# Performance work log

Hardware: AMD Instinct MI355X
Metric: run time of the kernel (lower is better)

Reference implementation:

```python
import jax, jax.numpy as jnp
import numpy as np

B, L, DIM = 8, 512, 8          # batch, seq len, raw channels (value dim D = 2*DIM = 16)
ET, HID, H = 128, 128, 2       # embed_time, hidden_size, num_heads
MAXLEN = 512
NEG = -1e9


def setup_inputs() -> dict:
    key = jax.random.key(0)
    ks = jax.random.split(key, 40)
    def n(i, shape, s=0.05):
        return jax.random.normal(ks[i], shape, jnp.float32) * s
    vals = jax.random.normal(ks[0], (B, L, DIM), jnp.float32)
    msk = (jax.random.uniform(ks[1], (B, L, DIM)) > 0.2).astype(jnp.float32)
    x = jnp.concatenate([vals, msk], -1)                      # (B, L, 2*DIM)
    time_steps = jax.random.uniform(ks[2], (B, L), jnp.float32)
    return {
        'x': x, 'time_steps': time_steps,
        # learned time embedding: Linear(1, ET-1) periodic + Linear(1,1)
        'w_per': n(3, (1, ET - 1)), 'b_per': n(4, (ET - 1,)),
        'w_lin': n(5, (1, 1)), 'b_lin': n(6, (1,)),
        # MultiTimeAttention projections
        'Wq_t': n(7, (ET, ET)), 'bq_t': n(8, (ET,)),
        'Wk_t': n(9, (ET, ET)), 'bk_t': n(10, (ET,)),
        'Wo_t': n(11, (2 * DIM * H, HID)), 'bo_t': n(12, (HID,)),
        'pos_emb': n(13, (MAXLEN + 1, HID)), 'cls_emb': n(14, (1, HID)),
        # transformer block (BERT-style post-LN encoder layer, d_ff=HID)
        'tWq': n(15, (HID, HID)), 'tbq': n(16, (HID,)),
        'tWk': n(17, (HID, HID)), 'tbk': n(18, (HID,)),
        'tWv': n(19, (HID, HID)), 'tbv': n(20, (HID,)),
        'tWo': n(21, (HID, HID)), 'tbo': n(22, (HID,)),
        'ln1_g': jnp.ones((HID,), jnp.float32), 'ln1_b': jnp.zeros((HID,), jnp.float32),
        'fW1': n(23, (HID, HID)), 'fb1': n(24, (HID,)),
        'fW2': n(25, (HID, HID)), 'fb2': n(26, (HID,)),
        'ln2_g': jnp.ones((HID,), jnp.float32), 'ln2_b': jnp.zeros((HID,), jnp.float32),
        # BertPooler
        'pW': n(27, (HID, HID)), 'pb': n(28, (HID,)),
    }


def _time_emb(tt, w_per, b_per, w_lin, b_lin):
    tt = tt[..., None]                                        # (B, L, 1)
    return jnp.concatenate([tt @ w_lin + b_lin, jnp.sin(tt @ w_per + b_per)], -1)


def _ln(x, g, b, eps=1e-5):
    m = x.mean(-1, keepdims=True)
    v = ((x - m) ** 2).mean(-1, keepdims=True)
    return (x - m) / jnp.sqrt(v + eps) * g + b


def _mta(q_emb, k_emb, value, mask, Wq, bq, Wk, bk, Wo, bo):
    # MultiTimeAttention: scores broadcast to value-channel axis, softmax over keys
    D = value.shape[-1]
    dk = ET // H
    def split(e, W, b):
        p = e @ W + b
        return p.reshape(e.shape[0], -1, H, dk).transpose(0, 2, 1, 3)
    q = split(q_emb, Wq, bq)                                  # (Bq, H, Lq, dk)
    k = split(k_emb, Wk, bk)                                  # (B,  H, Lk, dk)
    scores = jnp.matmul(q, k.swapaxes(-1, -2)) / jnp.sqrt(jnp.float32(dk))  # (B,H,Lq,Lk)
    s5 = jnp.where(mask[:, None, None, :, :] == 0, NEG, scores[..., None])  # (B,H,Lq,Lk,D)
    p = jax.nn.softmax(s5, axis=-2)
    out = jnp.einsum('bhqkd,bkd->bhqd', p, value)             # (B, H, Lq, D)
    Bv = value.shape[0]
    out = out.transpose(0, 2, 1, 3).reshape(Bv, -1, H * D)
    return out @ Wo + bo


def _tblock(x, tWq, tbq, tWk, tbk, tWv, tbv, tWo, tbo, ln1_g, ln1_b,
            fW1, fb1, fW2, fb2, ln2_g, ln2_b):
    Bq, Lq, _ = x.shape
    dk = HID // H
    def heads(W, b):
        return (x @ W + b).reshape(Bq, Lq, H, dk).transpose(0, 2, 1, 3)
    q, k, v = heads(tWq, tbq), heads(tWk, tbk), heads(tWv, tbv)
    a = jax.nn.softmax(jnp.matmul(q, k.swapaxes(-1, -2)) / jnp.sqrt(jnp.float32(dk)), -1)
    o = jnp.matmul(a, v).transpose(0, 2, 1, 3).reshape(Bq, Lq, HID) @ tWo + tbo
    x = _ln(x + o, ln1_g, ln1_b)
    f = jax.nn.relu(x @ fW1 + fb1) @ fW2 + fb2
    return _ln(x + f, ln2_g, ln2_b)


def reference(x, time_steps, w_per, b_per, w_lin, b_lin,
              Wq_t, bq_t, Wk_t, bk_t, Wo_t, bo_t, pos_emb, cls_emb,
              tWq, tbq, tWk, tbk, tWv, tbv, tWo, tbo, ln1_g, ln1_b,
              fW1, fb1, fW2, fb2, ln2_g, ln2_b, pW, pb):
    Bx = x.shape[0]
    mask_half = x[:, :, DIM:]
    mask = jnp.concatenate([mask_half, mask_half], -1)        # (B, L, 2*DIM)
    key_e = _time_emb(time_steps, w_per, b_per, w_lin, b_lin)
    tq_e = _time_emb(time_steps, w_per, b_per, w_lin, b_lin)  # query_time_steps=None -> same
    cls_t = jnp.linspace(0.0, 1.0, 128, dtype=jnp.float32)[None]
    cls_q_e = _time_emb(cls_t, w_per, b_per, w_lin, b_lin)    # (1, 128, ET)
    cls_out = _mta(cls_q_e, key_e, x, mask, Wq_t, bq_t, Wk_t, bk_t, Wo_t, bo_t)
    out = _mta(tq_e, key_e, x, mask, Wq_t, bq_t, Wk_t, bk_t, Wo_t, bo_t)
    tb = (tWq, tbq, tWk, tbk, tWv, tbv, tWo, tbo, ln1_g, ln1_b,
          fW1, fb1, fW2, fb2, ln2_g, ln2_b)
    cls_repr = jnp.broadcast_to(cls_emb[None, :, :], (Bx, 1, HID))
    # encode(cls_out, is_pooling=True), pooling='bert': no pos emb, take token 0
    h = _tblock(jnp.concatenate([cls_repr, cls_out], 1), *tb)
    cls_pooling = jnp.tanh(h[:, 0] @ pW + pb)                 # (B, HID)
    # encode(out, is_pooling=False) [pretrain path]: pos emb + transformer, drop CLS
    h2 = jnp.concatenate([cls_repr, out], 1)                  # (B, L+1, HID)
    h2 = h2 + pos_emb[:h2.shape[1]][None]
    h2 = _tblock(h2, *tb)
    last_hidden_state = h2[:, 1:]                             # (B, L, HID)
    return cls_pooling, last_hidden_state
```

## Files before the change

kernel.cpp:

```cpp
#include <hip/hip_runtime.h>
#include <hip/hip_bf16.h>
#include <math.h>


static constexpr int NM_ = 8 * 513;
static constexpr int NC_ = 8 * 129;
static constexpr int NT_ = NM_ + NC_;

using bf = __hip_bfloat16;
typedef __attribute__((ext_vector_type(8))) short bf16x8;
typedef __attribute__((ext_vector_type(4))) short bf16x4;
typedef __attribute__((ext_vector_type(4))) float floatx4;
typedef __attribute__((ext_vector_type(8))) unsigned short ushortx8;

__device__ __forceinline__ float wave_reduce_sum(float v) {
    #pragma unroll
    for (int off = 32; off >= 1; off >>= 1) v += __shfl_xor(v, off);
    return v;
}
__device__ __forceinline__ float wave_reduce_max(float v) {
    #pragma unroll
    for (int off = 32; off >= 1; off >>= 1) v = fmaxf(v, __shfl_xor(v, off));
    return v;
}
__device__ __forceinline__ float u2f(unsigned short u) {
    return __uint_as_float(((unsigned)u) << 16);
}
__device__ __forceinline__ unsigned short f2u(float f) {
    unsigned u = __float_as_uint(f);
    return (unsigned short)((u + 0x7FFF + ((u >> 16) & 1)) >> 16);
}
__device__ __forceinline__ bf16x8 join8(bf16x4 lo, bf16x4 hi) {
    return __builtin_shufflevector(lo, hi, 0, 1, 2, 3, 4, 5, 6, 7);
}
__device__ __forceinline__ float rdin(const void* p, int i, int flag) {
    return flag ? u2f(((const unsigned short*)p)[i]) : ((const float*)p)[i];
}

struct PrepAll {
    const void* src[32]; int n[32]; int dstoff[32];
    int cstart[32]; int cnum[32];
    int ncv;
    const void* wsrc[8]; unsigned short* wdst[8]; float wscale[8];
    const void* ts; const void* w_per; const void* b_per;
    const void* w_lin; const void* b_lin;
    unsigned short* key_e16;
    unsigned short* btg;
    const void* xsrc;
    const unsigned short* det;
};
__global__ void prep_all_kernel(PrepAll a, float* dst) {
    int flag = (a.det[0] == 0x3F80u) ? 1 : 0;
    int blk = blockIdx.x, tid = threadIdx.x;
    if (blk < a.ncv) {
        int which = -1, bi = 0;
        #pragma unroll
        for (int i = 0; i < 32; ++i)
            if (blk >= a.cstart[i] && blk < a.cstart[i] + a.cnum[i]) { which = i; bi = blk - a.cstart[i]; }
        if (which < 0) return;
        int i = bi * 256 + tid;
        if (i < a.n[which]) dst[a.dstoff[which] + i] = rdin(a.src[which], i, flag);
    } else if (blk < a.ncv + 512) {
        int p = blk - a.ncv;
        int m = p >> 6;
        int idx = (p & 63) * 256 + tid;
        int c = idx >> 9;
        int l = (idx >> 3) & 63;
        int j = idx & 7;
        int k = (c >> 3) * 32 + (l >> 4) * 8 + j;
        int n = (c & 7) * 16 + (l & 15);
        a.wdst[m][idx] = f2u(rdin(a.wsrc[m], k * 128 + n, flag) * a.wscale[m]);
    } else if (blk < a.ncv + 512 + 2112) {
        int p = blk - a.ncv - 512;
        int row = p * 2 + (tid >> 7), j = tid & 127;
        float t = (row < 4096) ? rdin(a.ts, row, flag)
                               : (float)(row - 4096) * (1.0f / 127.0f);
        float v;
        if (j == 0) v = t * rdin(a.w_lin, 0, flag) + rdin(a.b_lin, 0, flag);
        else        v = sinf(t * rdin(a.w_per, j - 1, flag) + rdin(a.b_per, j - 1, flag));
        a.key_e16[row * 128 + j] = f2u(v);
    } else {
        int p = blk - a.ncv - 512 - 2112;
        int e0 = (p * 256 + tid) * 8;
        int b = e0 >> 13;
        int c = (e0 >> 9) & 15;
        int k0 = e0 & 511;
        unsigned short out[8];
        #pragma unroll
        for (int j = 0; j < 8; ++j) {
            int k = k0 + j;
            float m = rdin(a.xsrc, (b * 512 + k) * 16 + 8 + (c & 7), flag);
            float val = (c < 8) ? rdin(a.xsrc, (b * 512 + k) * 16 + c, flag) * m : m;
            out[j] = f2u(val);
        }
        *(ushortx8*)(a.btg + e0) = *(ushortx8*)out;
    }
}

struct GemmM {
    const void* A[3]; const unsigned short* W[3]; const float* bias[3];
    unsigned short* C[3];
    int M[3]; float bscale[3];
};
__global__ void __launch_bounds__(256)
gemm_mfma_kernel(GemmM p) {
    int y = blockIdx.y;
    const unsigned short* Wsw = p.W[y];
    const float* bias = p.bias[y];
    unsigned short* C = p.C[y];
    int M = p.M[y];
    float bscale = p.bscale[y];
    int m0 = blockIdx.x * 16;
    if (m0 >= M) return;
    __shared__ unsigned short As[16][136];
    int tid = threadIdx.x;
    {
        const unsigned short* A = (const unsigned short*)p.A[y];
        int r = tid >> 4, c0 = (tid & 15) * 8;
        ushortx8 v = {0, 0, 0, 0, 0, 0, 0, 0};
        if (m0 + r < M) v = *(const ushortx8*)(A + (size_t)(m0 + r) * 128 + c0);
        *(ushortx8*)&As[r][c0] = v;
    }
    __syncthreads();

    int wv = tid >> 6, lane = tid & 63;
    floatx4 acc0 = {0.f, 0.f, 0.f, 0.f}, acc1 = acc0;
    int am = lane & 15, aq = lane >> 4;
    #pragma unroll
    for (int ks = 0; ks < 4; ++ks) {
        bf16x8 af = *(bf16x8*)&As[am][ks * 32 + aq * 8];
        const unsigned short* base = Wsw + ((size_t)ks * 8 + 2 * wv) * 512 + lane * 8;
        bf16x8 b0 = *(const bf16x8*)(base);
        bf16x8 b1 = *(const bf16x8*)(base + 512);
        acc0 = __builtin_amdgcn_mfma_f32_16x16x32_bf16(af, b0, acc0, 0, 0, 0);
        acc1 = __builtin_amdgcn_mfma_f32_16x16x32_bf16(af, b1, acc1, 0, 0, 0);
    }
    int col = lane & 15, rowb = (lane >> 4) * 4;
    #pragma unroll
    for (int t = 0; t < 2; ++t) {
        floatx4 acc = t ? acc1 : acc0;
        int n = wv * 32 + t * 16 + col;
        float bv = bias[n] * bscale;
        #pragma unroll
        for (int rg = 0; rg < 4; ++rg) {
            int m = m0 + rowb + rg;
            if (m < M) C[(size_t)m * 128 + n] = f2u(acc[rg] + bv);
        }
    }
}

__global__ void __launch_bounds__(256)
mta_att_kernel(const unsigned short* qp_cls, const unsigned short* qp_main,
               const unsigned short* kp, const unsigned short* btg,
               float* att_cls, float* att_mn) {
    int is_cls = (blockIdx.x >= 32);
    int qt = is_cls ? (blockIdx.x - 32) : blockIdx.x;
    int h = blockIdx.y, b = blockIdx.z;
    int tid = threadIdx.x, lane = tid & 63, wv = tid >> 6;
    __shared__ unsigned short Qs[16][72];
    __shared__ unsigned short KV[64][72];
    __shared__ unsigned short sp[16][520];
    int q0 = qt * 16;

    if (tid < 128) {
        int r = tid >> 3, c0 = (tid & 7) * 8;
        const unsigned short* qrow = is_cls ? (qp_cls + (size_t)(q0 + r) * 128 + h * 64)
                                            : (qp_main + (size_t)(b * 512 + q0 + r) * 128 + h * 64);
        *(ushortx8*)&Qs[r][c0] = *(const ushortx8*)(qrow + c0);
    }
    __syncthreads();

    bf16x8 qf0, qf1;
    {
        int m = lane & 15, g = lane >> 4;
        qf0 = *(const bf16x8*)&Qs[m][g * 8];
        qf1 = *(const bf16x8*)&Qs[m][32 + g * 8];
    }

    for (int kt = 0; kt < 8; ++kt) {
        int k0 = kt * 64;
        {
            int kk = tid >> 3, e0 = (tid & 7) * 8;
            #pragma unroll
            for (int it = 0; it < 2; ++it, kk += 32)
                *(ushortx8*)&KV[kk][e0] =
                    *(const ushortx8*)(kp + (size_t)(b * 512 + k0 + kk) * 128 + h * 64 + e0);
        }
        __syncthreads();
        int kn = lane & 15, g = lane >> 4;
        floatx4 acc = {0.f, 0.f, 0.f, 0.f};
        {
            bf16x8 b0 = *(const bf16x8*)&KV[wv * 16 + kn][g * 8];
            acc = __builtin_amdgcn_mfma_f32_16x16x32_bf16(qf0, b0, acc, 0, 0, 0);
            bf16x8 b1 = *(const bf16x8*)&KV[wv * 16 + kn][32 + g * 8];
            acc = __builtin_amdgcn_mfma_f32_16x16x32_bf16(qf1, b1, acc, 0, 0, 0);
        }
        int colk = k0 + wv * 16 + kn;
        #pragma unroll
        for (int rg = 0; rg < 4; ++rg) sp[g * 4 + rg][colk] = f2u(acc[rg]);
        __syncthreads();
    }

    for (int rr = wv; rr < 16; rr += 4) {
        float m = -1e30f;
        for (int k = lane; k < 512; k += 64) m = fmaxf(m, u2f(sp[rr][k]));
        m = wave_reduce_max(m);
        for (int k = lane; k < 512; k += 64) sp[rr][k] = f2u(expf(u2f(sp[rr][k]) - m));
    }
    __syncthreads();

    floatx4 macc = {0.f, 0.f, 0.f, 0.f};
    {
        int mq = lane & 15, g = lane >> 4;
        const unsigned short* bbase = btg + ((size_t)(b * 16 + mq)) * 512 + g * 8;
        #pragma unroll
        for (int cc = 0; cc < 4; ++cc) {
            int koff = (wv + cc * 4) * 32;
            bf16x8 af = *(const bf16x8*)&sp[mq][koff + g * 8];
            bf16x8 bfv = *(const bf16x8*)(bbase + koff);
            macc = __builtin_amdgcn_mfma_f32_16x16x32_bf16(af, bfv, macc, 0, 0, 0);
        }
    }
    float* redC = (float*)&KV[0][0];
    float* Cfull = redC + 1024;
    #pragma unroll
    for (int rg = 0; rg < 4; ++rg) redC[(wv * 64 + lane) * 4 + rg] = macc[rg];
    __syncthreads();
    {
        int l = tid >> 2, rg = tid & 3;
        float s = redC[l * 4 + rg] + redC[(64 + l) * 4 + rg]
                + redC[(128 + l) * 4 + rg] + redC[(192 + l) * 4 + rg];
        int row = (l >> 4) * 4 + rg, c = l & 15;
        Cfull[row * 16 + c] = s;
    }
    __syncthreads();
    if (tid < 128) {
        int r = tid >> 3, c = tid & 7;
        float num = Cfull[r * 16 + c];
        float den = Cfull[r * 16 + 8 + c];
        int row = q0 + r;
        float* dst = is_cls ? (att_cls + (size_t)(b * 128 + row) * 32)
                            : (att_mn + (size_t)(b * 512 + row) * 32);
        dst[h * 16 + c] = num / den;
        dst[h * 16 + 8 + c] = 1.0f;
    }
}

__global__ void __launch_bounds__(256)
mta_qkv_kernel(const float* att, const float* Wo, const float* bo,
               const float* cls_emb, const float* pos, float* xin,
               const unsigned short* Wq, const unsigned short* Wk, const unsigned short* Wv,
               const float* bq, const float* bk, const float* bv_,
               unsigned short* outq, unsigned short* outk, unsigned short* outv) {
    int m0 = blockIdx.x * 16;
    __shared__ float As32[16][36];
    __shared__ unsigned short As[16][136];
    int tid = threadIdx.x;
    int r = tid >> 4, g = tid & 15, c0 = g * 8;

    int R = m0 + r;
    int srow, prow;
    if (R < NM_) {
        int b = R / 513, rr = R - b * 513;
        srow = (rr == 0) ? -1 : 1024 + b * 512 + (rr - 1);
        prow = rr;
    } else {
        int mc = R - NM_;
        int b = mc / 129, rr = mc - b * 129;
        srow = (rr == 0) ? -1 : b * 128 + (rr - 1);
        prow = -1;
    }
    if (g < 2 && srow >= 0) {
        const float* src = att + (size_t)srow * 32 + g * 16;
        *(float4*)&As32[r][g * 16]      = *(const float4*)(src);
        *(float4*)&As32[r][g * 16 + 4]  = *(const float4*)(src + 4);
        *(float4*)&As32[r][g * 16 + 8]  = *(const float4*)(src + 8);
        *(float4*)&As32[r][g * 16 + 12] = *(const float4*)(src + 12);
    }
    __syncthreads();

    float acc[8];
    if (srow < 0) {
        #pragma unroll
        for (int j = 0; j < 8; ++j) acc[j] = cls_emb[c0 + j];
    } else {
        #pragma unroll
        for (int j = 0; j < 8; ++j) acc[j] = bo[c0 + j];
        #pragma unroll 8
        for (int k = 0; k < 32; ++k) {
            float a = As32[r][k];
            const float4 w0 = *(const float4*)(Wo + (size_t)k * 128 + c0);
            const float4 w1 = *(const float4*)(Wo + (size_t)k * 128 + c0 + 4);
            acc[0] = fmaf(a, w0.x, acc[0]); acc[1] = fmaf(a, w0.y, acc[1]);
            acc[2] = fmaf(a, w0.z, acc[2]); acc[3] = fmaf(a, w0.w, acc[3]);
            acc[4] = fmaf(a, w1.x, acc[4]); acc[5] = fmaf(a, w1.y, acc[5]);
            acc[6] = fmaf(a, w1.z, acc[6]); acc[7] = fmaf(a, w1.w, acc[7]);
        }
    }
    if (prow >= 0) {
        const float* pr = pos + (size_t)prow * 128 + c0;
        float4 p0 = *(const float4*)(pr);
        float4 p1 = *(const float4*)(pr + 4);
        acc[0] += p0.x; acc[1] += p0.y; acc[2] += p0.z; acc[3] += p0.w;
        acc[4] += p1.x; acc[5] += p1.y; acc[6] += p1.z; acc[7] += p1.w;
    }
    *(float4*)(xin + (size_t)R * 128 + c0) = make_float4(acc[0], acc[1], acc[2], acc[3]);
    *(float4*)(xin + (size_t)R * 128 + c0 + 4) = make_float4(acc[4], acc[5], acc[6], acc[7]);
    *(ushort4*)&As[r][c0] = make_ushort4(f2u(acc[0]), f2u(acc[1]), f2u(acc[2]), f2u(acc[3]));
    *(ushort4*)&As[r][c0 + 4] = make_ushort4(f2u(acc[4]), f2u(acc[5]), f2u(acc[6]), f2u(acc[7]));
    __syncthreads();

    int wv = tid >> 6, lane = tid & 63;
    int am = lane & 15, aq = lane >> 4;
    int col = lane & 15, rowb = (lane >> 4) * 4;
    const unsigned short* Ws[3] = {Wq, Wk, Wv};
    const float* bs[3] = {bq, bk, bv_};
    float bsc[3] = {0.125f, 1.f, 1.f};
    unsigned short* Cs[3] = {outq, outk, outv};
    #pragma unroll
    for (int y = 0; y < 3; ++y) {
        floatx4 acc0 = {0.f, 0.f, 0.f, 0.f}, acc1 = acc0;
        #pragma unroll
        for (int ks = 0; ks < 4; ++ks) {
            bf16x8 af = *(bf16x8*)&As[am][ks * 32 + aq * 8];
            const unsigned short* base = Ws[y] + ((size_t)ks * 8 + 2 * wv) * 512 + lane * 8;
            bf16x8 b0 = *(const bf16x8*)(base);
            bf16x8 b1 = *(const bf16x8*)(base + 512);
            acc0 = __builtin_amdgcn_mfma_f32_16x16x32_bf16(af, b0, acc0, 0, 0, 0);
            acc1 = __builtin_amdgcn_mfma_f32_16x16x32_bf16(af, b1, acc1, 0, 0, 0);
        }
        #pragma unroll
        for (int t = 0; t < 2; ++t) {
            floatx4 a2 = t ? acc1 : acc0;
            int n = wv * 32 + t * 16 + col;
            float bvv = bs[y][n] * bsc[y];
            #pragma unroll
            for (int rg = 0; rg < 4; ++rg)
                Cs[y][(size_t)(m0 + rowb + rg) * 128 + n] = f2u(a2[rg] + bvv);
        }
    }
}

__global__ void __launch_bounds__(256)
tb_att_kernel(const unsigned short* qp, const unsigned short* kp,
              const unsigned short* vp, unsigned short* outp) {
    int is_cls = (blockIdx.x >= 33);
    int qt = is_cls ? blockIdx.x - 33 : blockIdx.x;
    int h = blockIdx.y, b = blockIdx.z;
    int Lq = is_cls ? 129 : 513;
    int base = is_cls ? (4104 + b * 129) : (b * 513);
    int nkt = is_cls ? 3 : 9;
    int tid = threadIdx.x, lane = tid & 63, wv = tid >> 6;
    __shared__ unsigned short Qs[16][72];
    __shared__ unsigned short KV[64][72];
    __shared__ unsigned short sp[16][588];
    __shared__ float rinv[16];
    int q0 = qt * 16;

    if (tid < 128) {
        int r = tid >> 3, c0 = (tid & 7) * 8;
        int qr = q0 + r;
        ushortx8 v = {0, 0, 0, 0, 0, 0, 0, 0};
        if (qr < Lq) v = *(const ushortx8*)(qp + (size_t)(base + qr) * 128 + h * 64 + c0);
        *(ushortx8*)&Qs[r][c0] = v;
    }
    __syncthreads();

    bf16x8 qf0, qf1;
    {
        int m = lane & 15, g = lane >> 4;
        qf0 = *(const bf16x8*)&Qs[m][g * 8];
        qf1 = *(const bf16x8*)&Qs[m][32 + g * 8];
    }

    for (int kt = 0; kt < nkt; ++kt) {
        int k0 = kt * 64;
        {
            int kk = tid >> 3, e0 = (tid & 7) * 8;
            #pragma unroll
            for (int it = 0; it < 2; ++it, kk += 32) {
                int krow = k0 + kk;
                ushortx8 v = {0, 0, 0, 0, 0, 0, 0, 0};
                if (krow < Lq) v = *(const ushortx8*)(kp + (size_t)(base + krow) * 128 + h * 64 + e0);
                *(ushortx8*)&KV[kk][e0] = v;
            }
        }
        __syncthreads();
        int kn = lane & 15, g = lane >> 4;
        floatx4 acc = {0.f, 0.f, 0.f, 0.f};
        {
            bf16x8 b0 = *(const bf16x8*)&KV[wv * 16 + kn][g * 8];
            acc = __builtin_amdgcn_mfma_f32_16x16x32_bf16(qf0, b0, acc, 0, 0, 0);
            bf16x8 b1 = *(const bf16x8*)&KV[wv * 16 + kn][32 + g * 8];
            acc = __builtin_amdgcn_mfma_f32_16x16x32_bf16(qf1, b1, acc, 0, 0, 0);
        }
        int colk = k0 + wv * 16 + kn;
        #pragma unroll
        for (int rg = 0; rg < 4; ++rg)
            sp[g * 4 + rg][colk] = f2u((colk < Lq) ? acc[rg] : -1e30f);
        __syncthreads();
    }

    int kend = nkt * 64;
    for (int rr = wv; rr < 16; rr += 4) {
        float m = -1e30f;
        for (int k = lane; k < kend; k += 64) m = fmaxf(m, u2f(sp[rr][k]));
        m = wave_reduce_max(m);
        float sum = 0.f;
        for (int k = lane; k < kend; k += 64) {
            float e = expf(u2f(sp[rr][k]) - m);
            sp[rr][k] = f2u(e);
            sum += e;
        }
        sum = wave_reduce_sum(sum);
        if (lane == 0) rinv[rr] = 1.f / sum;
    }

    floatx4 oacc = {0.f, 0.f, 0.f, 0.f};
    for (int kt = 0; kt < nkt; ++kt) {
        int k0 = kt * 64;
        __syncthreads();
        {
            int kk = tid & 31, e0 = (tid >> 5) * 8;
            #pragma unroll
            for (int it = 0; it < 2; ++it, kk += 32) {
                int krow = k0 + kk;
                ushortx8 v = {0, 0, 0, 0, 0, 0, 0, 0};
                if (krow < Lq) v = *(const ushortx8*)(vp + (size_t)(base + krow) * 128 + h * 64 + e0);
                #pragma unroll
                for (int j = 0; j < 8; ++j) KV[e0 + j][kk] = v[j];
            }
        }
        __syncthreads();
        int dn = lane & 15, g = lane >> 4;
        #pragma unroll
        for (int c = 0; c < 2; ++c) {
            bf16x4 plo = *(const bf16x4*)&sp[lane & 15][k0 + c * 32 + g * 8];
            bf16x4 phi = *(const bf16x4*)&sp[lane & 15][k0 + c * 32 + g * 8 + 4];
            bf16x8 vf = *(const bf16x8*)&KV[wv * 16 + dn][c * 32 + g * 8];
            oacc = __builtin_amdgcn_mfma_f32_16x16x32_bf16(join8(plo, phi), vf, oacc, 0, 0, 0);
        }
    }
    int dcol = wv * 16 + (lane & 15), g = lane >> 4;
    #pragma unroll
    for (int rg = 0; rg < 4; ++rg) {
        int q = g * 4 + rg;
        int qr = q0 + q;
        if (qr < Lq)
            outp[(size_t)(base + qr) * 128 + h * 64 + dcol] = f2u(oacc[rg] * rinv[q]);
    }
}

__global__ void __launch_bounds__(256)
attnout_ffn_kernel(const unsigned short* A, const unsigned short* Wao, const float* bao,
                   const float* resid, const float* g1, const float* b1ln,
                   const unsigned short* W1, const float* fb1,
                   const unsigned short* W2, const float* fb2,
                   const float* g2, const float* b2ln,
                   const float* pW, const float* pb, float* dout) {
    int m0 = blockIdx.x * 16;
    __shared__ unsigned short As[16][136];
    __shared__ float Xs[16][128];
    __shared__ unsigned short Hs[16][136];
    __shared__ float redS[4][4][4], redQ[4][4][4];
    __shared__ float smean[16], sinv[16];
    __shared__ float x2row[128];
    __shared__ int poolb;
    int tid = threadIdx.x;
    if (tid == 0) poolb = -1;
    {
        int r = tid >> 4, c0 = (tid & 15) * 8;
        *(ushortx8*)&As[r][c0] = *(const ushortx8*)(A + (size_t)(m0 + r) * 128 + c0);
    }
    __syncthreads();

    int wv = tid >> 6, lane = tid & 63;
    int am = lane & 15, aq = lane >> 4;
    int col = lane & 15, g = lane >> 4, rowb = g * 4;

    float ov[2][4];
    {
        floatx4 acc0 = {0.f, 0.f, 0.f, 0.f}, acc1 = acc0;
        #pragma unroll
        for (int ks = 0; ks < 4; ++ks) {
            bf16x8 af = *(bf16x8*)&As[am][ks * 32 + aq * 8];
            const unsigned short* base = Wao + ((size_t)ks * 8 + 2 * wv) * 512 + lane * 8;
            bf16x8 bb0 = *(const bf16x8*)(base);
            bf16x8 bb1 = *(const bf16x8*)(base + 512);
            acc0 = __builtin_amdgcn_mfma_f32_16x16x32_bf16(af, bb0, acc0, 0, 0, 0);
            acc1 = __builtin_amdgcn_mfma_f32_16x16x32_bf16(af, bb1, acc1, 0, 0, 0);
        }
        #pragma unroll
        for (int t = 0; t < 2; ++t) {
            int n = wv * 32 + t * 16 + col;
            float bv = bao[n];
            floatx4 acc = t ? acc1 : acc0;
            #pragma unroll
            for (int rg = 0; rg < 4; ++rg)
                ov[t][rg] = acc[rg] + bv + resid[(size_t)(m0 + rowb + rg) * 128 + n];
        }
    }
    #pragma unroll
    for (int rg = 0; rg < 4; ++rg) {
        float s = ov[0][rg] + ov[1][rg];
        float q = ov[0][rg] * ov[0][rg] + ov[1][rg] * ov[1][rg];
        #pragma unroll
        for (int off = 8; off >= 1; off >>= 1) {
            s += __shfl_xor(s, off);
            q += __shfl_xor(q, off);
        }
        if ((lane & 15) == 0) { redS[wv][g][rg] = s; redQ[wv][g][rg] = q; }
    }
    __syncthreads();
    if (tid < 16) {
        int gg = tid >> 2, rg = tid & 3;
        float s = redS[0][gg][rg] + redS[1][gg][rg] + redS[2][gg][rg] + redS[3][gg][rg];
        float q = redQ[0][gg][rg] + redQ[1][gg][rg] + redQ[2][gg][rg] + redQ[3][gg][rg];
        float mean = s * 0.0078125f;
        float var = q * 0.0078125f - mean * mean;
        smean[tid] = mean;
        sinv[tid] = rsqrtf(var + 1e-5f);
    }
    __syncthreads();
    #pragma unroll
    for (int t = 0; t < 2; ++t) {
        int n = wv * 32 + t * 16 + col;
        float gm = g1[n], bb = b1ln[n];
        #pragma unroll
        for (int rg = 0; rg < 4; ++rg) {
            int row = rowb + rg;
            float val = (ov[t][rg] - smean[row]) * sinv[row] * gm + bb;
            Xs[row][n] = val;
            As[row][n] = f2u(val);
        }
    }
    __syncthreads();

    {
        floatx4 acc0 = {0.f, 0.f, 0.f, 0.f}, acc1 = acc0;
        #pragma unroll
        for (int ks = 0; ks < 4; ++ks) {
            bf16x8 af = *(bf16x8*)&As[am][ks * 32 + aq * 8];
            const unsigned short* base = W1 + ((size_t)ks * 8 + 2 * wv) * 512 + lane * 8;
            bf16x8 bb0 = *(const bf16x8*)(base);
            bf16x8 bb1 = *(const bf16x8*)(base + 512);
            acc0 = __builtin_amdgcn_mfma_f32_16x16x32_bf16(af, bb0, acc0, 0, 0, 0);
            acc1 = __builtin_amdgcn_mfma_f32_16x16x32_bf16(af, bb1, acc1, 0, 0, 0);
        }
        #pragma unroll
        for (int t = 0; t < 2; ++t) {
            int n = wv * 32 + t * 16 + col;
            float bv = fb1[n];
            floatx4 acc = t ? acc1 : acc0;
            #pragma unroll
            for (int rg = 0; rg < 4; ++rg)
                Hs[rowb + rg][n] = f2u(fmaxf(acc[rg] + bv, 0.f));
        }
    }
    __syncthreads();

    floatx4 acc0 = {0.f, 0.f, 0.f, 0.f}, acc1 = acc0;
    #pragma unroll
    for (int ks = 0; ks < 4; ++ks) {
        bf16x8 af = *(bf16x8*)&Hs[am][ks * 32 + aq * 8];
        const unsigned short* base = W2 + ((size_t)ks * 8 + 2 * wv) * 512 + lane * 8;
        bf16x8 bb0 = *(const bf16x8*)(base);
        bf16x8 bb1 = *(const bf16x8*)(base + 512);
        acc0 = __builtin_amdgcn_mfma_f32_16x16x32_bf16(af, bb0, acc0, 0, 0, 0);
        acc1 = __builtin_amdgcn_mfma_f32_16x16x32_bf16(af, bb1, acc1, 0, 0, 0);
    }
    #pragma unroll
    for (int t = 0; t < 2; ++t) {
        int n = wv * 32 + t * 16 + col;
        float bv = fb2[n];
        floatx4 acc = t ? acc1 : acc0;
        #pragma unroll
        for (int rg = 0; rg < 4; ++rg)
            ov[t][rg] = acc[rg] + bv + Xs[rowb + rg][n];
    }
    #pragma unroll
    for (int rg = 0; rg < 4; ++rg) {
        float s = ov[0][rg] + ov[1][rg];
        float q = ov[0][rg] * ov[0][rg] + ov[1][rg] * ov[1][rg];
        #pragma unroll
        for (int off = 8; off >= 1; off >>= 1) {
            s += __shfl_xor(s, off);
            q += __shfl_xor(q, off);
        }
        if ((lane & 15) == 0) { redS[wv][g][rg] = s; redQ[wv][g][rg] = q; }
    }
    __syncthreads();
    if (tid < 16) {
        int gg = tid >> 2, rg = tid & 3;
        float s = redS[0][gg][rg] + redS[1][gg][rg] + redS[2][gg][rg] + redS[3][gg][rg];
        float q = redQ[0][gg][rg] + redQ[1][gg][rg] + redQ[2][gg][rg] + redQ[3][gg][rg];
        float mean = s * 0.0078125f;
        float var = q * 0.0078125f - mean * mean;
        smean[tid] = mean;
        sinv[tid] = rsqrtf(var + 1e-5f);
    }
    __syncthreads();
    #pragma unroll
    for (int t = 0; t < 2; ++t) {
        int n = wv * 32 + t * 16 + col;
        float gm = g2[n], bb = b2ln[n];
        #pragma unroll
        for (int rg = 0; rg < 4; ++rg) {
            int row = rowb + rg;
            int m = m0 + row;
            float val = (ov[t][rg] - smean[row]) * sinv[row] * gm + bb;
            if (m < NM_) {
                int b = m / 513, r = m - b * 513;
                if (r >= 1)
                    dout[1024 + (size_t)b * 65536 + (size_t)(r - 1) * 128 + n] = val;
            } else {
                int mc = m - NM_;
                int b = mc / 129, r = mc - b * 129;
                if (r == 0) {
                    x2row[n] = val;
                    if (n == 0) poolb = b;
                }
            }
        }
    }
    __syncthreads();
    if (poolb >= 0 && tid < 128) {
        float acc = pb[tid];
        for (int k = 0; k < 128; ++k) acc = fmaf(x2row[k], pW[(size_t)k * 128 + tid], acc);
        dout[(size_t)poolb * 128 + tid] = tanhf(acc);
    }
}

extern "C" void kernel_launch(void* const* d_in, const int* in_sizes, int n_in,
                              void* d_out, int out_size, void* d_ws, size_t ws_size,
                              hipStream_t stream) {
    float* w = (float*)d_ws;
    size_t off = 0;
    auto alloc = [&](size_t n) {
        float* p = w + off;
        off += (n + 3) & ~(size_t)3;
        return p;
    };
    auto allocU = [&](size_t n) { return (unsigned short*)alloc((n + 1) / 2); };

    PrepAll pa{};
    int nn = n_in < 32 ? n_in : 32;
    float* fin[32];
    const int needconv[32] = {0,0,0,0,0,0, 0,1, 0,1, 1,1, 1,1, 0,1, 0,1, 0,1,
                              0,1, 1,1, 0,1, 0,1, 1,1, 1,1};
    int ncv = 0;
    for (int i = 0; i < nn; ++i) {
        pa.src[i] = d_in[i];
        pa.n[i] = in_sizes[i];
        fin[i] = alloc(in_sizes[i]);
        pa.dstoff[i] = (int)(fin[i] - w);
        if (needconv[i]) {
            int nb = (in_sizes[i] + 255) / 256;
            pa.cstart[i] = ncv;
            pa.cnum[i] = nb;
            ncv += nb;
        } else { pa.cstart[i] = -1; pa.cnum[i] = 0; }
    }
    for (int i = nn; i < 32; ++i) {
        pa.src[i] = nullptr; pa.n[i] = 0; pa.dstoff[i] = 0;
        pa.cstart[i] = -1; pa.cnum[i] = 0;
    }
    pa.ncv = ncv;

    const float* bq_t    = fin[7];
    const float* bk_t    = fin[9];
    const float* Wo_t    = fin[10]; const float* bo_t = fin[11];
    const float* pos_emb = fin[12]; const float* cls_emb = fin[13];
    const float* tbq = fin[15]; const float* tbk = fin[17]; const float* tbv = fin[19];
    const float* tbo = fin[21];
    const float* ln1_g = fin[22]; const float* ln1_b = fin[23];
    const float* fb1 = fin[25]; const float* fb2 = fin[27];
    const float* ln2_g = fin[28]; const float* ln2_b = fin[29];
    const float* pW = fin[30]; const float* pb = fin[31];

    const int widx[8] = {8, 6, 14, 16, 18, 20, 24, 26};
    unsigned short* wsw[8];
    for (int i = 0; i < 8; ++i) {
        wsw[i] = allocU(16384);
        pa.wsrc[i] = d_in[widx[i]];
        pa.wdst[i] = wsw[i];
        pa.wscale[i] = (i == 1 || i == 2) ? 0.125f : 1.0f;
    }
    pa.ts = d_in[1]; pa.w_per = d_in[2]; pa.b_per = d_in[3];
    pa.w_lin = d_in[4]; pa.b_lin = d_in[5];
    pa.xsrc = d_in[0];
    pa.det = (const unsigned short*)d_in[22];

    unsigned short* key_e16 = allocU(4224 * 128);
    unsigned short* cls_e16 = key_e16 + 4096 * 128;
    pa.key_e16 = key_e16;
    unsigned short* btg = allocU(8 * 16 * 512);
    pa.btg = btg;

    unsigned short* qp_main16 = allocU(4096 * 128);
    unsigned short* kp_main16 = allocU(4096 * 128);
    unsigned short* qp_cls16  = allocU(128 * 128);
    float* att_all = alloc(5120 * 32);
    float* att_cls = att_all;
    float* att_mn  = att_all + 1024 * 32;
    float* xin     = alloc((size_t)NT_ * 128);
    unsigned short* tbq16 = allocU((size_t)NT_ * 128);
    unsigned short* tbk16 = allocU((size_t)NT_ * 128);
    unsigned short* tbv16 = allocU((size_t)NT_ * 128);
    unsigned short* tba16 = allocU((size_t)NT_ * 128);
    (void)ws_size;

    float* outf = (float*)d_out;

    prep_all_kernel<<<ncv + 512 + 2112 + 32, 256, 0, stream>>>(pa, w);

    {
        GemmM p{};
        p.A[0] = key_e16; p.W[0] = wsw[0]; p.bias[0] = bk_t; p.C[0] = kp_main16;
        p.M[0] = 4096; p.bscale[0] = 1.f;
        p.A[1] = key_e16; p.W[1] = wsw[1]; p.bias[1] = bq_t; p.C[1] = qp_main16;
        p.M[1] = 4096; p.bscale[1] = 0.125f;
        p.A[2] = cls_e16; p.W[2] = wsw[1]; p.bias[2] = bq_t; p.C[2] = qp_cls16;
        p.M[2] = 128; p.bscale[2] = 0.125f;
        gemm_mfma_kernel<<<dim3(256, 3), 256, 0, stream>>>(p);
    }

    mta_att_kernel<<<dim3(40, 2, 8), 256, 0, stream>>>(qp_cls16, qp_main16, kp_main16,
                                                       btg, att_cls, att_mn);

    mta_qkv_kernel<<<321, 256, 0, stream>>>(att_all, Wo_t, bo_t, cls_emb, pos_emb, xin,
                                            wsw[2], wsw[3], wsw[4], tbq, tbk, tbv,
                                            tbq16, tbk16, tbv16);

    tb_att_kernel<<<dim3(42, 2, 8), 256, 0, stream>>>(tbq16, tbk16, tbv16, tba16);

    attnout_ffn_kernel<<<321, 256, 0, stream>>>(tba16, wsw[5], tbo, xin, ln1_g, ln1_b,
                                                wsw[6], fb1, wsw[7], fb2, ln2_g, ln2_b,
                                                pW, pb, outf);
}
```

Before: 180.4 us.

## Store V transposed and load MFMA operands directly from global memory

The QKV projection kernel now writes V transposed into a padded buffer, with a strided layout and zeroed tail columns set up in the prep kernel. The transformer attention kernel then reads V fragments straight from global memory instead of staging and transposing them through LDS. The GEMM, MTA attention and transformer attention kernels also load Q and K fragments directly from global memory, which removes the LDS staging and many __syncthreads per tile. In exchange, the transposed V write is a scattered, uncoalesced store, and the direct loads depend on cache hits rather than shared-memory reuse.

```diff
diff --git a/kernel.cpp b/kernel.cpp
--- a/kernel.cpp
+++ b/kernel.cpp
@@ -6,6 +6,7 @@
 static constexpr int NM_ = 8 * 513;
 static constexpr int NC_ = 8 * 129;
 static constexpr int NT_ = NM_ + NC_;
+static constexpr int VTS_ = 5248;
 
 using bf = __hip_bfloat16;
 typedef __attribute__((ext_vector_type(8))) short bf16x8;
@@ -47,6 +48,7 @@
     unsigned short* key_e16;
     unsigned short* btg;
     const void* xsrc;
+    unsigned short* vt;
     const unsigned short* det;
 };
 __global__ void prep_all_kernel(PrepAll a, float* dst) {
@@ -79,7 +81,7 @@
         if (j == 0) v = t * rdin(a.w_lin, 0, flag) + rdin(a.b_lin, 0, flag);
         else        v = sinf(t * rdin(a.w_per, j - 1, flag) + rdin(a.b_per, j - 1, flag));
         a.key_e16[row * 128 + j] = f2u(v);
-    } else {
+    } else if (blk < a.ncv + 512 + 2112 + 32) {
         int p = blk - a.ncv - 512 - 2112;
         int e0 = (p * 256 + tid) * 8;
         int b = e0 >> 13;
@@ -94,6 +96,12 @@
             out[j] = f2u(val);
         }
         *(ushortx8*)(a.btg + e0) = *(ushortx8*)out;
+    } else {
+        int p = blk - a.ncv - 512 - 2112 - 32;
+        int idx = p * 256 + tid;
+        int n = idx / 14, c8 = idx - n * 14;
+        ushortx8 z = {0, 0, 0, 0, 0, 0, 0, 0};
+        *(ushortx8*)(a.vt + (size_t)n * VTS_ + 5136 + c8 * 8) = z;
     }
 }
 
@@ -112,23 +120,15 @@
     float bscale = p.bscale[y];
     int m0 = blockIdx.x * 16;
     if (m0 >= M) return;
-    __shared__ unsigned short As[16][136];
     int tid = threadIdx.x;
-    {
-        const unsigned short* A = (const unsigned short*)p.A[y];
-        int r = tid >> 4, c0 = (tid & 15) * 8;
-        ushortx8 v = {0, 0, 0, 0, 0, 0, 0, 0};
-        if (m0 + r < M) v = *(const ushortx8*)(A + (size_t)(m0 + r) * 128 + c0);
-        *(ushortx8*)&As[r][c0] = v;
-    }
-    __syncthreads();
-
     int wv = tid >> 6, lane = tid & 63;
+    int am = lane & 15, aq = lane >> 4;
+    const unsigned short* A = (const unsigned short*)p.A[y];
+    const unsigned short* Arow = A + (size_t)(m0 + am) * 128;
     floatx4 acc0 = {0.f, 0.f, 0.f, 0.f}, acc1 = acc0;
-    int am = lane & 15, aq = lane >> 4;
     #pragma unroll
     for (int ks = 0; ks < 4; ++ks) {
-        bf16x8 af = *(bf16x8*)&As[am][ks * 32 + aq * 8];
+        bf16x8 af = *(const bf16x8*)(Arow + ks * 32 + aq * 8);
         const unsigned short* base = Wsw + ((size_t)ks * 8 + 2 * wv) * 512 + lane * 8;
         bf16x8 b0 = *(const bf16x8*)(base);
         bf16x8 b1 = *(const bf16x8*)(base + 512);
@@ -142,10 +142,8 @@
         int n = wv * 32 + t * 16 + col;
         float bv = bias[n] * bscale;
         #pragma unroll
-        for (int rg = 0; rg < 4; ++rg) {
-            int m = m0 + rowb + rg;
-            if (m < M) C[(size_t)m * 128 + n] = f2u(acc[rg] + bv);
-        }
+        for (int rg = 0; rg < 4; ++rg)
+            C[(size_t)(m0 + rowb + rg) * 128 + n] = f2u(acc[rg] + bv);
     }
 }
 
@@ -157,74 +155,54 @@
     int qt = is_cls ? (blockIdx.x - 32) : blockIdx.x;
     int h = blockIdx.y, b = blockIdx.z;
     int tid = threadIdx.x, lane = tid & 63, wv = tid >> 6;
-    __shared__ unsigned short Qs[16][72];
-    __shared__ unsigned short KV[64][72];
     __shared__ unsigned short sp[16][520];
+    __shared__ float red[1024 + 256];
     int q0 = qt * 16;
-
-    if (tid < 128) {
-        int r = tid >> 3, c0 = (tid & 7) * 8;
-        const unsigned short* qrow = is_cls ? (qp_cls + (size_t)(q0 + r) * 128 + h * 64)
-                                            : (qp_main + (size_t)(b * 512 + q0 + r) * 128 + h * 64);
-        *(ushortx8*)&Qs[r][c0] = *(const ushortx8*)(qrow + c0);
-    }
-    __syncthreads();
-
-    bf16x8 qf0, qf1;
-    {
-        int m = lane & 15, g = lane >> 4;
-        qf0 = *(const bf16x8*)&Qs[m][g * 8];
-        qf1 = *(const bf16x8*)&Qs[m][32 + g * 8];
-    }
-
+    int m = lane & 15, g = lane >> 4;
+
+    const unsigned short* qrow = is_cls ? (qp_cls + (size_t)(q0 + m) * 128 + h * 64)
+                                        : (qp_main + (size_t)(b * 512 + q0 + m) * 128 + h * 64);
+    bf16x8 qf0 = *(const bf16x8*)(qrow + g * 8);
+    bf16x8 qf1 = *(const bf16x8*)(qrow + 32 + g * 8);
+
+    const unsigned short* kbase = kp + ((size_t)b * 512) * 128 + h * 64;
+    #pragma unroll
     for (int kt = 0; kt < 8; ++kt) {
-        int k0 = kt * 64;
-        {
-            int kk = tid >> 3, e0 = (tid & 7) * 8;
-            #pragma unroll
-            for (int it = 0; it < 2; ++it, kk += 32)
-                *(ushortx8*)&KV[kk][e0] =
-                    *(const ushortx8*)(kp + (size_t)(b * 512 + k0 + kk) * 128 + h * 64 + e0);
-        }
-        __syncthreads();
-        int kn = lane & 15, g = lane >> 4;
+        int colk = kt * 64 + wv * 16 + m;
+        const unsigned short* kb = kbase + (size_t)colk * 128;
+        bf16x8 b0 = *(const bf16x8*)(kb + g * 8);
+        bf16x8 b1 = *(const bf16x8*)(kb + 32 + g * 8);
         floatx4 acc = {0.f, 0.f, 0.f, 0.f};
-        {
-            bf16x8 b0 = *(const bf16x8*)&KV[wv * 16 + kn][g * 8];
-            acc = __builtin_amdgcn_mfma_f32_16x16x32_bf16(qf0, b0, acc, 0, 0, 0);
-            bf16x8 b1 = *(const bf16x8*)&KV[wv * 16 + kn][32 + g * 8];
-            acc = __builtin_amdgcn_mfma_f32_16x16x32_bf16(qf1, b1, acc, 0, 0, 0);
-        }
-        int colk = k0 + wv * 16 + kn;
+        acc = __builtin_amdgcn_mfma_f32_16x16x32_bf16(qf0, b0, acc, 0, 0, 0);
+        acc = __builtin_amdgcn_mfma_f32_16x16x32_bf16(qf1, b1, acc, 0, 0, 0);
         #pragma unroll
         for (int rg = 0; rg < 4; ++rg) sp[g * 4 + rg][colk] = f2u(acc[rg]);
-        __syncthreads();
-    }
+    }
+    __syncthreads();
 
     for (int rr = wv; rr < 16; rr += 4) {
-        float m = -1e30f;
-        for (int k = lane; k < 512; k += 64) m = fmaxf(m, u2f(sp[rr][k]));
-        m = wave_reduce_max(m);
-        for (int k = lane; k < 512; k += 64) sp[rr][k] = f2u(expf(u2f(sp[rr][k]) - m));
+        float mx = -1e30f;
+        for (int k = lane; k < 512; k += 64) mx = fmaxf(mx, u2f(sp[rr][k]));
+        mx = wave_reduce_max(mx);
+        for (int k = lane; k < 512; k += 64) sp[rr][k] = f2u(expf(u2f(sp[rr][k]) - mx));
     }
     __syncthreads();
 
     floatx4 macc = {0.f, 0.f, 0.f, 0.f};
     {
-        int mq = lane & 15, g = lane >> 4;
-        const unsigned short* bbase = btg + ((size_t)(b * 16 + mq)) * 512 + g * 8;
+        const unsigned short* bbase = btg + ((size_t)(b * 16 + m)) * 512 + g * 8;
         #pragma unroll
         for (int cc = 0; cc < 4; ++cc) {
             int koff = (wv + cc * 4) * 32;
-            bf16x8 af = *(const bf16x8*)&sp[mq][koff + g * 8];
+            bf16x8 af = *(const bf16x8*)&sp[m][koff + g * 8];
             bf16x8 bfv = *(const bf16x8*)(bbase + koff);
             macc = __builtin_amdgcn_mfma_f32_16x16x32_bf16(af, bfv, macc, 0, 0, 0);
         }
     }
-    float* redC = (float*)&KV[0][0];
-    float* Cfull = redC + 1024;
-    #pragma unroll
-    for (int rg = 0; rg < 4; ++rg) redC[(wv * 64 + lane) * 4 + rg] = macc[rg];
+    float* redC = red;
+    float* Cfull = red + 1024;
+    #pragma unroll
+    for (int rg = 0; rg < 4; ++rg) redC[tid * 4 + rg] = macc[rg];
     __syncthreads();
     {
         int l = tid >> 2, rg = tid & 3;
@@ -251,7 +229,7 @@
                const float* cls_emb, const float* pos, float* xin,
                const unsigned short* Wq, const unsigned short* Wk, const unsigned short* Wv,
                const float* bq, const float* bk, const float* bv_,
-               unsigned short* outq, unsigned short* outk, unsigned short* outv) {
+               unsigned short* outq, unsigned short* outk, unsigned short* vT) {
     int m0 = blockIdx.x * 16;
     __shared__ float As32[16][36];
     __shared__ unsigned short As[16][136];
@@ -316,7 +294,7 @@
     const unsigned short* Ws[3] = {Wq, Wk, Wv};
     const float* bs[3] = {bq, bk, bv_};
     float bsc[3] = {0.125f, 1.f, 1.f};
-    unsigned short* Cs[3] = {outq, outk, outv};
+    unsigned short* Cs[2] = {outq, outk};
     #pragma unroll
     for (int y = 0; y < 3; ++y) {
         floatx4 acc0 = {0.f, 0.f, 0.f, 0.f}, acc1 = acc0;
@@ -335,15 +313,18 @@
             int n = wv * 32 + t * 16 + col;
             float bvv = bs[y][n] * bsc[y];
             #pragma unroll
-            for (int rg = 0; rg < 4; ++rg)
-                Cs[y][(size_t)(m0 + rowb + rg) * 128 + n] = f2u(a2[rg] + bvv);
+            for (int rg = 0; rg < 4; ++rg) {
+                unsigned short val = f2u(a2[rg] + bvv);
+                if (y < 2) Cs[y][(size_t)(m0 + rowb + rg) * 128 + n] = val;
+                else       vT[(size_t)n * VTS_ + (m0 + rowb + rg)] = val;
+            }
         }
     }
 }
 
 __global__ void __launch_bounds__(256)
 tb_att_kernel(const unsigned short* qp, const unsigned short* kp,
-              const unsigned short* vp, unsigned short* outp) {
+              const unsigned short* vT, unsigned short* outp) {
     int is_cls = (blockIdx.x >= 33);
     int qt = is_cls ? blockIdx.x - 33 : blockIdx.x;
     int h = blockIdx.y, b = blockIdx.z;
@@ -351,103 +332,66 @@
     int base = is_cls ? (4104 + b * 129) : (b * 513);
     int nkt = is_cls ? 3 : 9;
     int tid = threadIdx.x, lane = tid & 63, wv = tid >> 6;
-    __shared__ unsigned short Qs[16][72];
-    __shared__ unsigned short KV[64][72];
     __shared__ unsigned short sp[16][588];
     __shared__ float rinv[16];
     int q0 = qt * 16;
-
-    if (tid < 128) {
-        int r = tid >> 3, c0 = (tid & 7) * 8;
-        int qr = q0 + r;
-        ushortx8 v = {0, 0, 0, 0, 0, 0, 0, 0};
-        if (qr < Lq) v = *(const ushortx8*)(qp + (size_t)(base + qr) * 128 + h * 64 + c0);
-        *(ushortx8*)&Qs[r][c0] = v;
-    }
-    __syncthreads();
-
-    bf16x8 qf0, qf1;
-    {
-        int m = lane & 15, g = lane >> 4;
-        qf0 = *(const bf16x8*)&Qs[m][g * 8];
-        qf1 = *(const bf16x8*)&Qs[m][32 + g * 8];
-    }
-
+    int m = lane & 15, g = lane >> 4;
+
+    int qr = q0 + m; if (qr >= Lq) qr = Lq - 1;
+    const unsigned short* qrow = qp + (size_t)(base + qr) * 128 + h * 64;
+    bf16x8 qf0 = *(const bf16x8*)(qrow + g * 8);
+    bf16x8 qf1 = *(const bf16x8*)(qrow + 32 + g * 8);
+
+    for (int kt = 0; kt < nkt; ++kt) {
+        int colk = kt * 64 + wv * 16 + m;
+        int krow = (colk < Lq) ? colk : (Lq - 1);
+        const unsigned short* kb = kp + (size_t)(base + krow) * 128 + h * 64;
+        bf16x8 b0 = *(const bf16x8*)(kb + g * 8);
+        bf16x8 b1 = *(const bf16x8*)(kb + 32 + g * 8);
+        floatx4 acc = {0.f, 0.f, 0.f, 0.f};
+        acc = __builtin_amdgcn_mfma_f32_16x16x32_bf16(qf0, b0, acc, 0, 0, 0);
+        acc = __builtin_amdgcn_mfma_f32_16x16x32_bf16(qf1, b1, acc, 0, 0, 0);
+        #pragma unroll
+        for (int rg = 0; rg < 4; ++rg)
+            sp[g * 4 + rg][colk] = f2u((colk < Lq) ? acc[rg] : -1e30f);
+    }
+    __syncthreads();
+
+    int kend = nkt * 64;
+    for (int rr = wv; rr < 16; rr += 4) {
+        float mx = -1e30f;
+        for (int k = lane; k < kend; k += 64) mx = fmaxf(mx, u2f(sp[rr][k]));
+        mx = wave_reduce_max(mx);
+        float sum = 0.f;
+        for (int k = lane; k < kend; k += 64) {
+            float e = expf(u2f(sp[rr][k]) - mx);
+            sp[rr][k] = f2u(e);
+            sum += e;
+        }
+        sum = wave_reduce_sum(sum);
+        if (lane == 0) rinv[rr] = 1.f / sum;
+    }
+    __syncthreads();
+
+    floatx4 oacc = {0.f, 0.f, 0.f, 0.f};
+    const unsigned short* vbase = vT + (size_t)(h * 64 + wv * 16 + m) * VTS_ + base;
     for (int kt = 0; kt < nkt; ++kt) {
         int k0 = kt * 64;
-        {
-            int kk = tid >> 3, e0 = (tid & 7) * 8;
-            #pragma unroll
-            for (int it = 0; it < 2; ++it, kk += 32) {
-                int krow = k0 + kk;
-                ushortx8 v = {0, 0, 0, 0, 0, 0, 0, 0};
-                if (krow < Lq) v = *(const ushortx8*)(kp + (size_t)(base + krow) * 128 + h * 64 + e0);
-                *(ushortx8*)&KV[kk][e0] = v;
-            }
-        }
-        __syncthreads();
-        int kn = lane & 15, g = lane >> 4;
-        floatx4 acc = {0.f, 0.f, 0.f, 0.f};
-        {
-            bf16x8 b0 = *(const bf16x8*)&KV[wv * 16 + kn][g * 8];
-            acc = __builtin_amdgcn_mfma_f32_16x16x32_bf16(qf0, b0, acc, 0, 0, 0);
-            bf16x8 b1 = *(const bf16x8*)&KV[wv * 16 + kn][32 + g * 8];
-            acc = __builtin_amdgcn_mfma_f32_16x16x32_bf16(qf1, b1, acc, 0, 0, 0);
-        }
-        int colk = k0 + wv * 16 + kn;
-        #pragma unroll
-        for (int rg = 0; rg < 4; ++rg)
-            sp[g * 4 + rg][colk] = f2u((colk < Lq) ? acc[rg] : -1e30f);
-        __syncthreads();
-    }
-
-    int kend = nkt * 64;
-    for (int rr = wv; rr < 16; rr += 4) {
-        float m = -1e30f;
-        for (int k = lane; k < kend; k += 64) m = fmaxf(m, u2f(sp[rr][k]));
-        m = wave_reduce_max(m);
-        float sum = 0.f;
-        for (int k = lane; k < kend; k += 64) {
-            float e = expf(u2f(sp[rr][k]) - m);
-            sp[rr][k] = f2u(e);
-            sum += e;
-        }
-        sum = wave_reduce_sum(sum);
-        if (lane == 0) rinv[rr] = 1.f / sum;
-    }
-
-    floatx4 oacc = {0.f, 0.f, 0.f, 0.f};
-    for (int kt = 0; kt < nkt; ++kt) {
-        int k0 = kt * 64;
-        __syncthreads();
-        {
-            int kk = tid & 31, e0 = (tid >> 5) * 8;
-            #pragma unroll
-            for (int it = 0; it < 2; ++it, kk += 32) {
-                int krow = k0 + kk;
-                ushortx8 v = {0, 0, 0, 0, 0, 0, 0, 0};
-                if (krow < Lq) v = *(const ushortx8*)(vp + (size_t)(base + krow) * 128 + h * 64 + e0);
-                #pragma unroll
-                for (int j = 0; j < 8; ++j) KV[e0 + j][kk] = v[j];
-            }
-        }
-        __syncthreads();
-        int dn = lane & 15, g = lane >> 4;
         #pragma unroll
         for (int c = 0; c < 2; ++c) {
-            bf16x4 plo = *(const bf16x4*)&sp[lane & 15][k0 + c * 32 + g * 8];
-            bf16x4 phi = *(const bf16x4*)&sp[lane & 15][k0 + c * 32 + g * 8 + 4];
-            bf16x8 vf = *(const bf16x8*)&KV[wv * 16 + dn][c * 32 + g * 8];
+            bf16x4 plo = *(const bf16x4*)&sp[m][k0 + c * 32 + g * 8];
+            bf16x4 phi = *(const bf16x4*)&sp[m][k0 + c * 32 + g * 8 + 4];
+            bf16x8 vf = *(const bf16x8*)(vbase + k0 + c * 32 + g * 8);
             oacc = __builtin_amdgcn_mfma_f32_16x16x32_bf16(join8(plo, phi), vf, oacc, 0, 0, 0);
         }
     }
-    int dcol = wv * 16 + (lane & 15), g = lane >> 4;
+    int dcol = wv * 16 + m;
     #pragma unroll
     for (int rg = 0; rg < 4; ++rg) {
         int q = g * 4 + rg;
-        int qr = q0 + q;
-        if (qr < Lq)
-            outp[(size_t)(base + qr) * 128 + h * 64 + dcol] = f2u(oacc[rg] * rinv[q]);
+        int qout = q0 + q;
+        if (qout < Lq)
+            outp[(size_t)(base + qout) * 128 + h * 64 + dcol] = f2u(oacc[rg] * rinv[q]);
     }
 }
 
@@ -706,13 +650,14 @@
     float* xin     = alloc((size_t)NT_ * 128);
     unsigned short* tbq16 = allocU((size_t)NT_ * 128);
     unsigned short* tbk16 = allocU((size_t)NT_ * 128);
-    unsigned short* tbv16 = allocU((size_t)NT_ * 128);
+    unsigned short* vT    = allocU((size_t)128 * VTS_);
     unsigned short* tba16 = allocU((size_t)NT_ * 128);
+    pa.vt = vT;
     (void)ws_size;
 
     float* outf = (float*)d_out;
 
-    prep_all_kernel<<<ncv + 512 + 2112 + 32, 256, 0, stream>>>(pa, w);
+    prep_all_kernel<<<ncv + 512 + 2112 + 32 + 7, 256, 0, stream>>>(pa, w);
 
     {
         GemmM p{};
@@ -730,9 +675,9 @@
 
     mta_qkv_kernel<<<321, 256, 0, stream>>>(att_all, Wo_t, bo_t, cls_emb, pos_emb, xin,
                                             wsw[2], wsw[3], wsw[4], tbq, tbk, tbv,
-                                            tbq16, tbk16, tbv16);
-
-    tb_att_kernel<<<dim3(42, 2, 8), 256, 0, stream>>>(tbq16, tbk16, tbv16, tba16);
+                                            tbq16, tbk16, vT);
+
+    tb_att_kernel<<<dim3(42, 2, 8), 256, 0, stream>>>(tbq16, tbk16, vT, tba16);
 
     attnout_ffn_kernel<<<321, 256, 0, stream>>>(tba16, wsw[5], tbo, xin, ln1_g, ln1_b,
                                                 wsw[6], fb1, wsw[7], fb2, ln2_g, ln2_b,
```

Result: slower. 188.2 us (+4.3%).
